# Optimization experiments

Measured on AMD Instinct MI355X. Metric: run time of the kernel, lower is better.

Reference implementation:

```python
import jax, jax.numpy as jnp
import numpy as np

OBS_LEN = 8
B = 262144
H = 16   # lstm hidden / MADE hidden / cond dim
D = 2    # trajectory input dim / flow dim
N_FLOWS = 4
CLAMP = 5.0


def _masks():
    # MADE masks for num_inputs=2, num_hidden=16 (ikostrikov get_mask)
    in_deg = jnp.arange(D) % D                      # [0, 1]
    hid_deg = jnp.zeros((H,), jnp.float32)          # arange(16) % (2-1) == 0
    out_deg = (jnp.arange(2 * D) % D - 1).astype(jnp.float32)  # [-1,0,-1,0]
    input_mask = (hid_deg[:, None] >= in_deg[None, :].astype(jnp.float32)).astype(jnp.float32)  # [16,2]
    hidden_mask = jnp.ones((H, H), jnp.float32)     # all degrees 0 -> full
    output_mask = (out_deg[:, None] >= hid_deg[None, :]).astype(jnp.float32)  # [4,16]
    return input_mask, hidden_mask, output_mask


def _made_ma(x, cond, p, masks):
    # x: [B,2], cond: [B,16] -> m, a: [B,2]
    im, hm, om = masks
    jW, jb, cW, hW, hb, oW, ob = p
    h = x @ (jW * im).T + jb + cond @ cW.T      # joiner (masked) + cond linear (no bias)
    h = jax.nn.relu(h)
    h = jax.nn.relu(h @ (hW * hm).T + hb)       # trunk hidden masked linear
    out = h @ (oW * om).T + ob                  # trunk output masked linear -> [B,4]
    m, a = out[:, :D], out[:, D:]
    a = CLAMP * jnp.tanh(a / CLAMP)             # soft log-scale clamp (clamp_flow)
    return m, a


def _made_inverse(u, cond, p, masks):
    x = jnp.zeros_like(u)
    for i in range(D):
        m, a = _made_ma(x, cond, p, masks)
        x = x.at[:, i].set(u[:, i] * jnp.exp(a[:, i]) + m[:, i])
    return x


def _maf_sample(noise, cond, made_params, masks):
    # modules = [MADE0,Rev,MADE1,Rev,MADE2,Rev,MADE3,Rev]; sample runs inverse in reversed order
    x = noise
    for k in reversed(range(N_FLOWS)):
        x = x[:, ::-1]                           # Reverse(2) inverse == flip
        p = tuple(t[k] for t in made_params)
        x = _made_inverse(x, cond, p, masks)
    return x


def _encode(traj, enc_W, enc_b, W_ih, W_hh, b_ih, b_hh, h0, c0):
    # obs_len LSTM loop; dropout is identity in eval/test mode
    def step(carry, x_t):
        h, c = carry
        e = jax.nn.relu(x_t @ enc_W.T + enc_b)                 # [B,16]
        g = e @ W_ih.T + b_ih + h @ W_hh.T + b_hh              # [B,64]
        i, f, gg, o = jnp.split(g, 4, axis=-1)                 # torch LSTMCell gate order
        c = jax.nn.sigmoid(f) * c + jax.nn.sigmoid(i) * jnp.tanh(gg)
        h = jax.nn.sigmoid(o) * jnp.tanh(c)
        return (h, c), None
    (h, c), _ = jax.lax.scan(step, (h0, c0), traj)
    return h


def setup_inputs() -> dict:
    key = jax.random.key(0)
    ks = jax.random.split(key, 16)
    s = 0.1
    return {
        "traj_rel": jax.random.normal(ks[0], (OBS_LEN + 1, B, D), jnp.float32),
        "obs_traj_pos": jax.random.normal(ks[1], (OBS_LEN, B, D), jnp.float32),
        "h0": jax.random.normal(ks[2], (B, H), jnp.float32),
        "c0": jax.random.normal(ks[3], (B, H), jnp.float32),
        "noise": jax.random.normal(ks[4], (B, D), jnp.float32),
        "enc_W": jax.random.normal(ks[5], (H, D), jnp.float32) * 0.2,
        "enc_b": jnp.zeros((H,), jnp.float32),
        "lstm_W_ih": jax.random.normal(ks[6], (4 * H, H), jnp.float32) * s,
        "lstm_W_hh": jax.random.normal(ks[7], (4 * H, H), jnp.float32) * 0.001,
        "lstm_b_ih": jnp.zeros((4 * H,), jnp.float32).at[H:2 * H].set(1.0),
        "lstm_b_hh": jnp.zeros((4 * H,), jnp.float32),
        "made_joiner_W": jax.random.normal(ks[8], (N_FLOWS, H, D), jnp.float32) * s,
        "made_joiner_b": jnp.zeros((N_FLOWS, H), jnp.float32),
        "made_cond_W": jax.random.normal(ks[9], (N_FLOWS, H, H), jnp.float32) * s,
        "made_hid_W": jax.random.normal(ks[10], (N_FLOWS, H, H), jnp.float32) * s,
        "made_hid_b": jnp.zeros((N_FLOWS, H), jnp.float32),
        "made_out_W": jax.random.normal(ks[11], (N_FLOWS, 2 * D, H), jnp.float32) * s,
        "made_out_b": jnp.zeros((N_FLOWS, 2 * D), jnp.float32),
    }


def reference(traj_rel, obs_traj_pos, h0, c0, noise,
              enc_W, enc_b, lstm_W_ih, lstm_W_hh, lstm_b_ih, lstm_b_hh,
              made_joiner_W, made_joiner_b, made_cond_W,
              made_hid_W, made_hid_b, made_out_W, made_out_b):
    masks = _masks()
    h = _encode(traj_rel[:OBS_LEN], enc_W, enc_b,
                lstm_W_ih, lstm_W_hh, lstm_b_ih, lstm_b_hh, h0, c0)  # [B,16]
    made_params = (made_joiner_W, made_joiner_b, made_cond_W,
                   made_hid_W, made_hid_b, made_out_W, made_out_b)
    goal = _maf_sample(noise, h, made_params, masks)                  # [B,2]
    return goal + obs_traj_pos[-1]                                    # mode='test' output_pred
```

## Files before the change

kernel.cpp:

```cpp
#include <hip/hip_runtime.h>

#define B_N 262144
#define OBS_N 8

typedef __attribute__((ext_vector_type(4))) _Float16 f16x4;
typedef __attribute__((ext_vector_type(2))) __fp16 fp16x2;
typedef __attribute__((ext_vector_type(4))) float f32x4;

#define LOG2E 1.44269504088896340736f

__device__ __forceinline__ float rcpf_(float x){ return __builtin_amdgcn_rcpf(x); }
__device__ __forceinline__ float exp2f_(float x){ return __builtin_amdgcn_exp2f(x); }
__device__ __forceinline__ float expf_(float x){ return exp2f_(LOG2E * x); }
__device__ __forceinline__ float sigm_(float x){ return rcpf_(1.0f + exp2f_(-LOG2E * x)); }
__device__ __forceinline__ float tanh_(float x){ return fmaf(-2.0f, rcpf_(exp2f_((2.0f*LOG2E) * x) + 1.0f), 1.0f); }

__device__ __forceinline__ f16x4 pack4(float a, float b, float c, float d){
    fp16x2 lo = __builtin_amdgcn_cvt_pkrtz(a, b);
    fp16x2 hi = __builtin_amdgcn_cvt_pkrtz(c, d);
    f16x4 r;
    r[0] = (_Float16)lo[0]; r[1] = (_Float16)lo[1];
    r[2] = (_Float16)hi[0]; r[3] = (_Float16)hi[1];
    return r;
}

#define MFMA16(a, b, c) __builtin_amdgcn_mfma_f32_16x16x16f16((a), (b), (c), 0, 0, 0)


__global__ __launch_bounds__(256) void goal_kernel(
    const float* __restrict__ traj,
    const float* __restrict__ obsp,
    const float* __restrict__ h0,
    const float* __restrict__ c0,
    const float* __restrict__ noise,
    const float* __restrict__ encW,
    const float* __restrict__ encb,
    const float* __restrict__ Wih,
    const float* __restrict__ Whh,
    const float* __restrict__ bih,
    const float* __restrict__ bhh,
    const float* __restrict__ jW,
    const float* __restrict__ jb,
    const float* __restrict__ cW,
    const float* __restrict__ hW,
    const float* __restrict__ hb,
    const float* __restrict__ oW,
    const float* __restrict__ ob,
    float* __restrict__ out)
{
    const int lane = threadIdx.x & 63;
    const int wv   = threadIdx.x >> 6;
    const int q    = lane >> 4;
    const int s    = lane & 15;
    const int j4   = q * 4;
    const int base = blockIdx.x * 128 + wv * 32;
    const int colA = base + s;
    const int colB = base + 16 + s;

    float ew0[4], ew1[4], eb[4];
    #pragma unroll
    for (int r = 0; r < 4; ++r) {
        ew0[r] = encW[(j4 + r) * 2 + 0];
        ew1[r] = encW[(j4 + r) * 2 + 1];
        eb[r]  = encb[j4 + r];
    }

    f16x4 wihA[4], whhA[4];
    f32x4 bias[4];
    #pragma unroll
    for (int m = 0; m < 4; ++m) {
        float4 wa = *(const float4*)(Wih + (16 * m + s) * 16 + j4);
        float4 wb = *(const float4*)(Whh + (16 * m + s) * 16 + j4);
        wihA[m] = pack4(wa.x, wa.y, wa.z, wa.w);
        whhA[m] = pack4(wb.x, wb.y, wb.z, wb.w);
        float4 b1 = *(const float4*)(bih + 16 * m + j4);
        float4 b2 = *(const float4*)(bhh + 16 * m + j4);
        f32x4 bv; bv[0] = b1.x + b2.x; bv[1] = b1.y + b2.y; bv[2] = b1.z + b2.z; bv[3] = b1.w + b2.w;
        bias[m] = bv;
    }

    f32x4 cA = *(const f32x4*)(c0 + colA * 16 + j4);
    f32x4 cB = *(const f32x4*)(c0 + colB * 16 + j4);
    float4 hA0 = *(const float4*)(h0 + colA * 16 + j4);
    float4 hB0 = *(const float4*)(h0 + colB * 16 + j4);
    f16x4 hA = pack4(hA0.x, hA0.y, hA0.z, hA0.w);
    f16x4 hB = pack4(hB0.x, hB0.y, hB0.z, hB0.w);

    float2 nzA = *(const float2*)(noise + colA * 2);
    float2 nzB = *(const float2*)(noise + colB * 2);

    float2 xA = *(const float2*)(traj + colA * 2);
    float2 xB = *(const float2*)(traj + colB * 2);

    for (int t = 0; t < OBS_N; ++t) {
        float2 nxA, nxB;
        if (t < OBS_N - 1) {
            nxA = *(const float2*)(traj + (t + 1) * (B_N * 2) + colA * 2);
            nxB = *(const float2*)(traj + (t + 1) * (B_N * 2) + colB * 2);
        }
        float eAv[4], eBv[4];
        #pragma unroll
        for (int r = 0; r < 4; ++r) {
            eAv[r] = fmaxf(fmaf(ew0[r], xA.x, fmaf(ew1[r], xA.y, eb[r])), 0.0f);
            eBv[r] = fmaxf(fmaf(ew0[r], xB.x, fmaf(ew1[r], xB.y, eb[r])), 0.0f);
        }
        f16x4 eA = pack4(eAv[0], eAv[1], eAv[2], eAv[3]);
        f16x4 eB = pack4(eBv[0], eBv[1], eBv[2], eBv[3]);

        f32x4 gA[4], gB[4];
        #pragma unroll
        for (int m = 0; m < 4; ++m) {
            gA[m] = MFMA16(wihA[m], eA, bias[m]);
            gA[m] = MFMA16(whhA[m], hA, gA[m]);
            gB[m] = MFMA16(wihA[m], eB, bias[m]);
            gB[m] = MFMA16(whhA[m], hB, gB[m]);
        }

        float hnA[4], hnB[4];
        #pragma unroll
        for (int r = 0; r < 4; ++r) {
            float cn = fmaf(sigm_(gA[1][r]), cA[r], sigm_(gA[0][r]) * tanh_(gA[2][r]));
            cA[r] = cn;
            hnA[r] = sigm_(gA[3][r]) * tanh_(cn);
            float cm = fmaf(sigm_(gB[1][r]), cB[r], sigm_(gB[0][r]) * tanh_(gB[2][r]));
            cB[r] = cm;
            hnB[r] = sigm_(gB[3][r]) * tanh_(cm);
        }
        hA = pack4(hnA[0], hnA[1], hnA[2], hnA[3]);
        hB = pack4(hnB[0], hnB[1], hnB[2], hnB[3]);

        if (t < OBS_N - 1) { xA = nxA; xB = nxB; }
    }

    float2 ppA = *(const float2*)(obsp + (OBS_N - 1) * (B_N * 2) + colA * 2);
    float2 ppB = *(const float2*)(obsp + (OBS_N - 1) * (B_N * 2) + colB * 2);

    float x0A = nzA.x, x1A = nzA.y;
    float x0B = nzB.x, x1B = nzB.y;

    #pragma unroll
    for (int kf = 3; kf >= 0; --kf) {
        float tA = x0A; x0A = x1A; x1A = tA;
        float tB = x0B; x0B = x1B; x1B = tB;

        float4 cw = *(const float4*)(cW + kf * 256 + s * 16 + j4);
        f16x4 cwA = pack4(cw.x, cw.y, cw.z, cw.w);
        float4 hw = *(const float4*)(hW + kf * 256 + s * 16 + j4);
        f16x4 hwA = pack4(hw.x, hw.y, hw.z, hw.w);
        int orow = (s < 4) ? s : 0;
        float4 ow = *(const float4*)(oW + kf * 64 + orow * 16 + j4);
        f16x4 owA;
        if (s < 4) owA = pack4(ow.x, ow.y, ow.z, ow.w);
        else { owA[0] = (_Float16)0.f; owA[1] = (_Float16)0.f; owA[2] = (_Float16)0.f; owA[3] = (_Float16)0.f; }

        float jw0[4], jb_[4], hb_[4];
        #pragma unroll
        for (int r = 0; r < 4; ++r) {
            jw0[r] = jW[kf * 32 + (j4 + r) * 2];
            jb_[r] = jb[kf * 16 + j4 + r];
            hb_[r] = hb[kf * 16 + j4 + r];
        }
        float ob0 = ob[kf * 4 + 0], ob1 = ob[kf * 4 + 1];
        float ob2 = ob[kf * 4 + 2], ob3 = ob[kf * 4 + 3];

        float ea0 = expf_(5.0f * tanh_(ob2 * 0.2f));
        x0A = fmaf(x0A, ea0, ob0);
        x0B = fmaf(x0B, ea0, ob0);

        f32x4 a1A, a1B;
        #pragma unroll
        for (int r = 0; r < 4; ++r) {
            a1A[r] = fmaf(jw0[r], x0A, jb_[r]);
            a1B[r] = fmaf(jw0[r], x0B, jb_[r]);
        }
        a1A = MFMA16(cwA, hA, a1A);
        a1B = MFMA16(cwA, hB, a1B);
        f16x4 h1A = pack4(fmaxf(a1A[0],0.f), fmaxf(a1A[1],0.f), fmaxf(a1A[2],0.f), fmaxf(a1A[3],0.f));
        f16x4 h1B = pack4(fmaxf(a1B[0],0.f), fmaxf(a1B[1],0.f), fmaxf(a1B[2],0.f), fmaxf(a1B[3],0.f));

        f32x4 a2A, a2B;
        #pragma unroll
        for (int r = 0; r < 4; ++r) { a2A[r] = hb_[r]; a2B[r] = hb_[r]; }
        a2A = MFMA16(hwA, h1A, a2A);
        a2B = MFMA16(hwA, h1B, a2B);
        f16x4 h2A = pack4(fmaxf(a2A[0],0.f), fmaxf(a2A[1],0.f), fmaxf(a2A[2],0.f), fmaxf(a2A[3],0.f));
        f16x4 h2B = pack4(fmaxf(a2B[0],0.f), fmaxf(a2B[1],0.f), fmaxf(a2B[2],0.f), fmaxf(a2B[3],0.f));

        f32x4 a3A, a3B;
        if (q == 0) { a3A[0]=ob0; a3A[1]=ob1; a3A[2]=ob2; a3A[3]=ob3;
                      a3B[0]=ob0; a3B[1]=ob1; a3B[2]=ob2; a3B[3]=ob3; }
        else        { a3A[0]=0.f; a3A[1]=0.f; a3A[2]=0.f; a3A[3]=0.f;
                      a3B[0]=0.f; a3B[1]=0.f; a3B[2]=0.f; a3B[3]=0.f; }
        a3A = MFMA16(owA, h2A, a3A);
        a3B = MFMA16(owA, h2B, a3B);

        float a1vA = 5.0f * tanh_(a3A[3] * 0.2f);
        float a1vB = 5.0f * tanh_(a3B[3] * 0.2f);
        float x1nA = fmaf(x1A, expf_(a1vA), a3A[1]);
        float x1nB = fmaf(x1B, expf_(a1vB), a3B[1]);
        x1A = __int_as_float(__builtin_amdgcn_ds_bpermute(s << 2, __float_as_int(x1nA)));
        x1B = __int_as_float(__builtin_amdgcn_ds_bpermute(s << 2, __float_as_int(x1nB)));
    }

    if (lane < 16) {
        float2 oA; oA.x = x0A + ppA.x; oA.y = x1A + ppA.y;
        float2 oB; oB.x = x0B + ppB.x; oB.y = x1B + ppB.y;
        *(float2*)(out + colA * 2) = oA;
        *(float2*)(out + colB * 2) = oB;
    }
}

extern "C" void kernel_launch(void* const* d_in, const int* in_sizes, int n_in,
                              void* d_out, int out_size, void* d_ws, size_t ws_size,
                              hipStream_t stream) {
    goal_kernel<<<B_N / 128, 256, 0, stream>>>(
        (const float*)d_in[0],  (const float*)d_in[1],  (const float*)d_in[2],
        (const float*)d_in[3],  (const float*)d_in[4],  (const float*)d_in[5],
        (const float*)d_in[6],  (const float*)d_in[7],  (const float*)d_in[8],
        (const float*)d_in[9],  (const float*)d_in[10], (const float*)d_in[11],
        (const float*)d_in[12], (const float*)d_in[13], (const float*)d_in[14],
        (const float*)d_in[15], (const float*)d_in[16], (const float*)d_in[17],
        (float*)d_out);
}
```

Baseline: 54.91 us.

## Fold activation scales into LSTM weights and share reciprocals in gate math

Pre-scales LSTM gate weights and biases by -log2e factors so sigmoid/tanh become raw exp2 calls, then combines the gate divisions into two reciprocals per element. Hoists per-flow output bias and constant exp computations out of the flow loop. Replicates the MADE output weight rows across all MFMA rows so every lane group gets the flow outputs directly, removing the ds_bpermute broadcast. Risks overflow in the combined products for large gate pre-activations and slightly different rounding from fp16 pre-scaled weights.

```diff
diff --git a/kernel.cpp b/kernel.cpp
--- a/kernel.cpp
+++ b/kernel.cpp
@@ -12,7 +12,6 @@
 __device__ __forceinline__ float rcpf_(float x){ return __builtin_amdgcn_rcpf(x); }
 __device__ __forceinline__ float exp2f_(float x){ return __builtin_amdgcn_exp2f(x); }
 __device__ __forceinline__ float expf_(float x){ return exp2f_(LOG2E * x); }
-__device__ __forceinline__ float sigm_(float x){ return rcpf_(1.0f + exp2f_(-LOG2E * x)); }
 __device__ __forceinline__ float tanh_(float x){ return fmaf(-2.0f, rcpf_(exp2f_((2.0f*LOG2E) * x) + 1.0f), 1.0f); }
 
 __device__ __forceinline__ f16x4 pack4(float a, float b, float c, float d){
@@ -65,18 +64,32 @@
         eb[r]  = encb[j4 + r];
     }
 
+    const float gsc[4] = { -LOG2E, -LOG2E, -2.0f*LOG2E, -LOG2E };
+
     f16x4 wihA[4], whhA[4];
     f32x4 bias[4];
     #pragma unroll
     for (int m = 0; m < 4; ++m) {
         float4 wa = *(const float4*)(Wih + (16 * m + s) * 16 + j4);
         float4 wb = *(const float4*)(Whh + (16 * m + s) * 16 + j4);
-        wihA[m] = pack4(wa.x, wa.y, wa.z, wa.w);
-        whhA[m] = pack4(wb.x, wb.y, wb.z, wb.w);
+        wihA[m] = pack4(wa.x*gsc[m], wa.y*gsc[m], wa.z*gsc[m], wa.w*gsc[m]);
+        whhA[m] = pack4(wb.x*gsc[m], wb.y*gsc[m], wb.z*gsc[m], wb.w*gsc[m]);
         float4 b1 = *(const float4*)(bih + 16 * m + j4);
         float4 b2 = *(const float4*)(bhh + 16 * m + j4);
-        f32x4 bv; bv[0] = b1.x + b2.x; bv[1] = b1.y + b2.y; bv[2] = b1.z + b2.z; bv[3] = b1.w + b2.w;
+        f32x4 bv;
+        bv[0] = (b1.x + b2.x)*gsc[m]; bv[1] = (b1.y + b2.y)*gsc[m];
+        bv[2] = (b1.z + b2.z)*gsc[m]; bv[3] = (b1.w + b2.w)*gsc[m];
         bias[m] = bv;
+    }
+
+    float ob0c[4], ob1c[4], ob2c[4], ob3c[4], ea0c[4];
+    #pragma unroll
+    for (int kf = 0; kf < 4; ++kf) {
+        ob0c[kf] = ob[kf*4 + 0];
+        ob1c[kf] = ob[kf*4 + 1];
+        ob2c[kf] = ob[kf*4 + 2];
+        ob3c[kf] = ob[kf*4 + 3] * 0.2f;
+        ea0c[kf] = expf_(5.0f * tanh_(ob2c[kf] * 0.2f));
     }
 
     f32x4 cA = *(const f32x4*)(c0 + colA * 16 + j4);
@@ -92,6 +105,8 @@
     float2 xA = *(const float2*)(traj + colA * 2);
     float2 xB = *(const float2*)(traj + colB * 2);
 
+    const float NEG2L2E = -2.0f * LOG2E;
+
     for (int t = 0; t < OBS_N; ++t) {
         float2 nxA, nxB;
         if (t < OBS_N - 1) {
@@ -119,12 +134,34 @@
         float hnA[4], hnB[4];
         #pragma unroll
         for (int r = 0; r < 4; ++r) {
-            float cn = fmaf(sigm_(gA[1][r]), cA[r], sigm_(gA[0][r]) * tanh_(gA[2][r]));
-            cA[r] = cn;
-            hnA[r] = sigm_(gA[3][r]) * tanh_(cn);
-            float cm = fmaf(sigm_(gB[1][r]), cB[r], sigm_(gB[0][r]) * tanh_(gB[2][r]));
-            cB[r] = cm;
-            hnB[r] = sigm_(gB[3][r]) * tanh_(cm);
+            {
+                float Ei = exp2f_(gA[0][r]);
+                float Ef = exp2f_(gA[1][r]);
+                float Eg = exp2f_(gA[2][r]);
+                float Eo = exp2f_(gA[3][r]);
+                float pi = 1.0f + Ei, pf = 1.0f + Ef, pg = 1.0f + Eg;
+                float m_ = pi * pg;
+                float R1 = rcpf_(m_ * pf);
+                float cn = fmaf(cA[r], m_, (1.0f - Eg) * pf) * R1;
+                cA[r] = cn;
+                float Ec = exp2f_(NEG2L2E * cn);
+                float R2 = rcpf_((1.0f + Ec) * (1.0f + Eo));
+                hnA[r] = (1.0f - Ec) * R2;
+            }
+            {
+                float Ei = exp2f_(gB[0][r]);
+                float Ef = exp2f_(gB[1][r]);
+                float Eg = exp2f_(gB[2][r]);
+                float Eo = exp2f_(gB[3][r]);
+                float pi = 1.0f + Ei, pf = 1.0f + Ef, pg = 1.0f + Eg;
+                float m_ = pi * pg;
+                float R1 = rcpf_(m_ * pf);
+                float cn = fmaf(cB[r], m_, (1.0f - Eg) * pf) * R1;
+                cB[r] = cn;
+                float Ec = exp2f_(NEG2L2E * cn);
+                float R2 = rcpf_((1.0f + Ec) * (1.0f + Eo));
+                hnB[r] = (1.0f - Ec) * R2;
+            }
         }
         hA = pack4(hnA[0], hnA[1], hnA[2], hnA[3]);
         hB = pack4(hnB[0], hnB[1], hnB[2], hnB[3]);
@@ -147,11 +184,11 @@
         f16x4 cwA = pack4(cw.x, cw.y, cw.z, cw.w);
         float4 hw = *(const float4*)(hW + kf * 256 + s * 16 + j4);
         f16x4 hwA = pack4(hw.x, hw.y, hw.z, hw.w);
-        int orow = (s < 4) ? s : 0;
-        float4 ow = *(const float4*)(oW + kf * 64 + orow * 16 + j4);
-        f16x4 owA;
-        if (s < 4) owA = pack4(ow.x, ow.y, ow.z, ow.w);
-        else { owA[0] = (_Float16)0.f; owA[1] = (_Float16)0.f; owA[2] = (_Float16)0.f; owA[3] = (_Float16)0.f; }
+        {
+        }
+        float osc = ((s & 3) == 3) ? 0.2f : 1.0f;
+        float4 ow = *(const float4*)(oW + kf * 64 + (s & 3) * 16 + j4);
+        f16x4 owA = pack4(ow.x * osc, ow.y * osc, ow.z * osc, ow.w * osc);
 
         float jw0[4], jb_[4], hb_[4];
         #pragma unroll
@@ -160,12 +197,9 @@
             jb_[r] = jb[kf * 16 + j4 + r];
             hb_[r] = hb[kf * 16 + j4 + r];
         }
-        float ob0 = ob[kf * 4 + 0], ob1 = ob[kf * 4 + 1];
-        float ob2 = ob[kf * 4 + 2], ob3 = ob[kf * 4 + 3];
-
-        float ea0 = expf_(5.0f * tanh_(ob2 * 0.2f));
-        x0A = fmaf(x0A, ea0, ob0);
-        x0B = fmaf(x0B, ea0, ob0);
+
+        x0A = fmaf(x0A, ea0c[kf], ob0c[kf]);
+        x0B = fmaf(x0B, ea0c[kf], ob0c[kf]);
 
         f32x4 a1A, a1B;
         #pragma unroll
@@ -187,22 +221,18 @@
         f16x4 h2B = pack4(fmaxf(a2B[0],0.f), fmaxf(a2B[1],0.f), fmaxf(a2B[2],0.f), fmaxf(a2B[3],0.f));
 
         f32x4 a3A, a3B;
-        if (q == 0) { a3A[0]=ob0; a3A[1]=ob1; a3A[2]=ob2; a3A[3]=ob3;
-                      a3B[0]=ob0; a3B[1]=ob1; a3B[2]=ob2; a3B[3]=ob3; }
-        else        { a3A[0]=0.f; a3A[1]=0.f; a3A[2]=0.f; a3A[3]=0.f;
-                      a3B[0]=0.f; a3B[1]=0.f; a3B[2]=0.f; a3B[3]=0.f; }
+        a3A[0]=ob0c[kf]; a3A[1]=ob1c[kf]; a3A[2]=ob2c[kf]; a3A[3]=ob3c[kf];
+        a3B[0]=ob0c[kf]; a3B[1]=ob1c[kf]; a3B[2]=ob2c[kf]; a3B[3]=ob3c[kf];
         a3A = MFMA16(owA, h2A, a3A);
         a3B = MFMA16(owA, h2B, a3B);
 
-        float a1vA = 5.0f * tanh_(a3A[3] * 0.2f);
-        float a1vB = 5.0f * tanh_(a3B[3] * 0.2f);
-        float x1nA = fmaf(x1A, expf_(a1vA), a3A[1]);
-        float x1nB = fmaf(x1B, expf_(a1vB), a3B[1]);
-        x1A = __int_as_float(__builtin_amdgcn_ds_bpermute(s << 2, __float_as_int(x1nA)));
-        x1B = __int_as_float(__builtin_amdgcn_ds_bpermute(s << 2, __float_as_int(x1nB)));
-    }
-
-    if (lane < 16) {
+        float a1vA = 5.0f * tanh_(a3A[3]);
+        float a1vB = 5.0f * tanh_(a3B[3]);
+        x1A = fmaf(x1A, expf_(a1vA), a3A[1]);
+        x1B = fmaf(x1B, expf_(a1vB), a3B[1]);
+    }
+
+    if (q == 0) {
         float2 oA; oA.x = x0A + ppA.x; oA.y = x1A + ppA.y;
         float2 oB; oB.x = x0B + ppB.x; oB.y = x1B + ppB.y;
         *(float2*)(out + colA * 2) = oA;
```

Result: faster. 50.22 us (-8.5%).
